# Performance work log

Measured on AMD Instinct MI355X. Metric: run time of the kernel, lower is better.

Reference implementation:

```python
import jax, jax.numpy as jnp
import numpy as np
from math import sqrt

DIM = 256
HEADS = 4
GROUPS = min(DIM // 4, 32)  # = 32
EPS = 1e-6


def setup_inputs() -> dict:
    key = jax.random.key(0)
    ks = jax.random.split(key, 10)
    B, C, H, W = 16, DIM, 32, 32
    x = jax.random.normal(ks[0], (B, C, H, W), dtype=jnp.float32)
    s = 1.0 / sqrt(C)
    inp = {
        'x': x,
        'gn_scale': jnp.ones((C,), jnp.float32),
        'gn_bias': jnp.zeros((C,), jnp.float32),
        'Wq': jax.random.normal(ks[1], (C, C), jnp.float32) * s,
        'bq': jnp.zeros((C,), jnp.float32),
        'Wk': jax.random.normal(ks[2], (C, C), jnp.float32) * s,
        'bk': jnp.zeros((C,), jnp.float32),
        'Wv': jax.random.normal(ks[3], (C, C), jnp.float32) * s,
        'bv': jnp.zeros((C,), jnp.float32),
        'Wp': jax.random.normal(ks[4], (C, C), jnp.float32) * s,
        'bp': jnp.zeros((C,), jnp.float32),
    }
    return inp


def _group_norm(x, scale, bias):
    B, C, H, W = x.shape
    xg = x.reshape(B, GROUPS, C // GROUPS, H, W)
    mean = xg.mean(axis=(2, 3, 4), keepdims=True)
    var = xg.var(axis=(2, 3, 4), keepdims=True)
    xg = (xg - mean) * jax.lax.rsqrt(var + EPS)
    x = xg.reshape(B, C, H, W)
    return x * scale[None, :, None, None] + bias[None, :, None, None]


def _lin_ch(x, W, b):
    # 1x1 conv / linear over channel dim: (B,C,H,W) x (C,Cout) -> (B,Cout,H,W)
    return jnp.einsum('bchw,cd->bdhw', x, W) + b[None, :, None, None]


def reference(x, gn_scale, gn_bias, Wq, bq, Wk, bk, Wv, bv, Wp, bp):
    B, C, H, W = x.shape
    dh = C // HEADS
    _x = _group_norm(x, gn_scale, gn_bias)
    q = _lin_ch(_x, Wq, bq).reshape(B, HEADS, dh, H, W)
    k = _lin_ch(_x, Wk, bk).reshape(B, HEADS, dh, H, W)
    v = _lin_ch(_x, Wv, bv).reshape(B, HEADS, dh, H, W)
    scores = jnp.einsum('bhdxy,bhdij->bhxyij', q, k) / sqrt(C)
    scores = scores.reshape(B, HEADS, H, W, H * W)
    weights = jax.nn.softmax(scores, axis=-1).reshape(B, HEADS, H, W, H, W)
    h = jnp.einsum('bhxyij,bhdij->bhdxy', weights, v).reshape(B, C, H, W)
    h = _lin_ch(h, Wp, bp)
    ret = (x + h) / sqrt(2.0)
    return ret
```

## Files before the change

kernel.cpp:

```cpp
#include <hip/hip_runtime.h>
#include <hip/hip_bf16.h>

#define BATCH 16
#define CH    256
#define HW    1024
#define NH    4
#define DH    64
#define NG    32
#define CPG   8
#define EPSV  1e-6f

#define QSCALE 0.090168440055558706f

typedef __bf16 bf16x8 __attribute__((ext_vector_type(8)));
typedef float  f32x4  __attribute__((ext_vector_type(4)));

__device__ __forceinline__ unsigned short f2bf(float f) {
    union { __hip_bfloat16 h; unsigned short u; } cv;
    cv.h = __float2bfloat16(f);
    return cv.u;
}

__device__ __forceinline__ unsigned int fbits(float f) {
    union { float f; unsigned int u; } cv; cv.f = f; return cv.u;
}

__device__ __forceinline__ void gld_lds16(const unsigned short* g, unsigned short* l) {
    __builtin_amdgcn_global_load_lds(
        (const __attribute__((address_space(1))) void*)g,
        (__attribute__((address_space(3))) void*)l, 16, 0, 0);
}

__global__ void prep_gn_kernel(const float* Wq, const float* Wk, const float* Wv,
                               const float* Wp, const float* bq, const float* bk,
                               const float* bv, unsigned short* wqkv_t,
                               unsigned short* wp_t, float* bqkv,
                               const float* x, const float* scale, const float* bias,
                               unsigned short* xn) {
    int t = threadIdx.x;
    if (blockIdx.x < 1024) {
        int idx = blockIdx.x * 256 + t;
        if (idx < 768 * 256) {
            int n = idx >> 8, c = idx & 255;
            const float* W = (n < 256) ? Wq : (n < 512) ? Wk : Wv;
            int d = n & 255;
            wqkv_t[idx] = f2bf(W[c * 256 + d]);
        } else {
            int j = idx - 768 * 256;
            int n = j >> 8, c = j & 255;
            wp_t[j] = f2bf(Wp[c * 256 + n]);
        }
        if (idx < 768)
            bqkv[idx] = (idx < 256) ? bq[idx] : (idx < 512) ? bk[idx - 256] : bv[idx - 512];
    } else {
        int bg = blockIdx.x - 1024;
        const float4* p = reinterpret_cast<const float4*>(x + (size_t)bg * (CPG * HW));
        float va[8][4];
        float s = 0.f, ss = 0.f;
#pragma unroll
        for (int k = 0; k < 8; k++) {
            float4 v = p[t + 256 * k];
            va[k][0] = v.x; va[k][1] = v.y; va[k][2] = v.z; va[k][3] = v.w;
            s += v.x + v.y + v.z + v.w;
            ss += v.x * v.x + v.y * v.y + v.z * v.z + v.w * v.w;
        }
        for (int o = 32; o; o >>= 1) { s += __shfl_down(s, o); ss += __shfl_down(ss, o); }
        __shared__ float as_[4], ass_[4];
        __shared__ float sA[8], sB[8];
        int w = t >> 6;
        if ((t & 63) == 0) { as_[w] = s; ass_[w] = ss; }
        __syncthreads();
        if (t < 8) {
            float S = as_[0] + as_[1] + as_[2] + as_[3];
            float SS = ass_[0] + ass_[1] + ass_[2] + ass_[3];
            float mean = S / (float)(CPG * HW);
            float var = SS / (float)(CPG * HW) - mean * mean;
            float rstd = rsqrtf(var + EPSV);
            int g = bg & 31;
            int c = g * CPG + t;
            float a = rstd * scale[c];
            sA[t] = a;
            sB[t] = bias[c] - mean * a;
        }
        __syncthreads();
        int b = bg >> 5, g = bg & 31;
        unsigned short* dst = xn + ((size_t)b * HW + t * 4) * CH + g * CPG;
#pragma unroll
        for (int pl = 0; pl < 4; pl++) {
            union { bf16x8 v8; __hip_bfloat162 h2[4]; } u;
#pragma unroll
            for (int c2 = 0; c2 < 4; c2++) {
                float v0 = fmaf(va[2 * c2][pl],     sA[2 * c2],     sB[2 * c2]);
                float v1 = fmaf(va[2 * c2 + 1][pl], sA[2 * c2 + 1], sB[2 * c2 + 1]);
                u.h2[c2] = __float22bfloat162_rn(float2{v0, v1});
            }
            *reinterpret_cast<bf16x8*>(dst + (size_t)pl * CH) = u.v8;
        }
    }
}

__global__ __launch_bounds__(256) void qkv_kernel(const unsigned short* xn,
        const unsigned short* wqkv_t, const float* bqkv,
        unsigned short* qb, unsigned short* kb, unsigned short* vb) {
    int t = threadIdx.x;
    int wv = t >> 6, lane = t & 63, quad = lane >> 4, ln = lane & 15;
    int wr = wv >> 1, wc = wv & 1;
    int m0 = blockIdx.x * 128 + wr * 64;
    int n0 = blockIdx.y * 128 + wc * 64;

    f32x4 acc[4][4] = {};
    for (int k0 = 0; k0 < CH; k0 += 32) {
        int koff = k0 + quad * 8;
        bf16x8 af[4], bfr[4];
#pragma unroll
        for (int i = 0; i < 4; i++)
            af[i] = *reinterpret_cast<const bf16x8*>(
                xn + (size_t)(m0 + i * 16 + ln) * CH + koff);
#pragma unroll
        for (int j = 0; j < 4; j++)
            bfr[j] = *reinterpret_cast<const bf16x8*>(
                wqkv_t + (size_t)(n0 + j * 16 + ln) * CH + koff);
#pragma unroll
        for (int i = 0; i < 4; i++)
#pragma unroll
            for (int j = 0; j < 4; j++)
                acc[i][j] = __builtin_amdgcn_mfma_f32_16x16x32_bf16(af[i], bfr[j], acc[i][j], 0, 0, 0);
    }
#pragma unroll
    for (int j = 0; j < 4; j++) {
        int n = n0 + j * 16 + ln;
        float bias = bqkv[n];
        int which = n >> 8;
        int dh_ = n & 255;
        int head = dh_ >> 6, d = dh_ & 63;
#pragma unroll
        for (int i = 0; i < 4; i++) {
            int mb = m0 + i * 16 + quad * 4;
            int bi = mb >> 10, p = mb & 1023;
            int bh = bi * NH + head;
            if (which < 2) {
                unsigned short* dst = (which == 0 ? qb : kb) + (size_t)bh * HW * DH;
                float sc = (which == 0) ? QSCALE : 1.0f;
#pragma unroll
                for (int r = 0; r < 4; r++)
                    dst[(size_t)(p + r) * DH + d] = f2bf((acc[i][j][r] + bias) * sc);
            } else {
                unsigned short* dst = vb + ((size_t)bh * DH + d) * HW + p;
                ushort4 pk4;
                pk4.x = f2bf(acc[i][j][0] + bias);
                pk4.y = f2bf(acc[i][j][1] + bias);
                pk4.z = f2bf(acc[i][j][2] + bias);
                pk4.w = f2bf(acc[i][j][3] + bias);
                *reinterpret_cast<ushort4*>(dst) = pk4;
            }
        }
    }
}

__global__ __launch_bounds__(256) void attn_kernel(const unsigned short* qb,
        const unsigned short* kb, const unsigned short* vb, unsigned short* h_t) {
    int qblk = blockIdx.x, bh = blockIdx.y;
    int t = threadIdx.x;
    int wv = t >> 6, lane = t & 63, quad = lane >> 4, ln = lane & 15;
    int q0 = qblk * 128 + wv * 32;

    const unsigned short* Q = qb + (size_t)bh * HW * DH;
    const unsigned short* K = kb + (size_t)bh * HW * DH;
    const unsigned short* V = vb + (size_t)bh * DH * HW;

    __shared__ __align__(16) unsigned short kbuf[2][4096];
    __shared__ __align__(16) unsigned short vbuf[2][4096];
    __shared__ __align__(16) unsigned short pbuf[4][2][16][72];

    int c_a = wv * 64 + lane;
    int c_b = 256 + wv * 64 + lane;
    int pa = c_a >> 3, ja = (c_a & 7) ^ (pa & 7);
    int pb = c_b >> 3, jb = (c_b & 7) ^ (pb & 7);
    const unsigned short* pka = K + (size_t)pa * DH + ja * 8;
    const unsigned short* pkb = K + (size_t)pb * DH + jb * 8;
    const unsigned short* pva = V + (size_t)pa * HW + ja * 8;
    const unsigned short* pvb = V + (size_t)pb * HW + jb * 8;
    int lofs_a = wv * 512, lofs_b = 2048 + wv * 512;

    int koffs[4][2];
#pragma unroll
    for (int mt = 0; mt < 4; mt++) {
        int p = mt * 16 + ln, sw = p & 7;
#pragma unroll
        for (int kk = 0; kk < 2; kk++)
            koffs[mt][kk] = p * 64 + (((kk * 4 + quad) ^ sw) * 8);
    }

    bf16x8 qf[2][2];
#pragma unroll
    for (int nq = 0; nq < 2; nq++)
#pragma unroll
        for (int kk = 0; kk < 2; kk++)
            qf[nq][kk] = *reinterpret_cast<const bf16x8*>(
                Q + (size_t)(q0 + nq * 16 + ln) * DH + kk * 32 + quad * 8);

    f32x4 ls[2] = {};
    f32x4 o[2][4] = {};

    gld_lds16(pka, &kbuf[0][lofs_a]);
    gld_lds16(pkb, &kbuf[0][lofs_b]);
    gld_lds16(pva, &vbuf[0][lofs_a]);
    gld_lds16(pvb, &vbuf[0][lofs_b]);
    pka += 64 * DH; pkb += 64 * DH; pva += 64; pvb += 64;

#define ATTN_TILE(B, DO_STAGE)                                                      \
    {                                                                               \
        __syncthreads();                                                            \
        if (DO_STAGE) {                                                             \
            gld_lds16(pka, &kbuf[B ^ 1][lofs_a]);                                   \
            gld_lds16(pkb, &kbuf[B ^ 1][lofs_b]);                                   \
            gld_lds16(pva, &vbuf[B ^ 1][lofs_a]);                                   \
            gld_lds16(pvb, &vbuf[B ^ 1][lofs_b]);                                   \
            pka += 64 * DH; pkb += 64 * DH; pva += 64; pvb += 64;                   \
        }                                                                           \
        bf16x8 kf[4][2], vf[4][2];                                                  \
        _Pragma("unroll")                                                           \
        for (int mt = 0; mt < 4; mt++) {                                            \
            _Pragma("unroll")                                                       \
            for (int kk = 0; kk < 2; kk++) {                                        \
                kf[mt][kk] = *reinterpret_cast<const bf16x8*>(&kbuf[B][koffs[mt][kk]]); \
                vf[mt][kk] = *reinterpret_cast<const bf16x8*>(&vbuf[B][koffs[mt][kk]]); \
            }                                                                       \
        }                                                                           \
        f32x4 s[2][4] = {};                                                         \
        _Pragma("unroll")                                                           \
        for (int nq = 0; nq < 2; nq++)                                              \
            _Pragma("unroll")                                                       \
            for (int mt = 0; mt < 4; mt++) {                                        \
                s[nq][mt] = __builtin_amdgcn_mfma_f32_16x16x32_bf16(kf[mt][0], qf[nq][0], s[nq][mt], 0, 0, 0); \
                s[nq][mt] = __builtin_amdgcn_mfma_f32_16x16x32_bf16(kf[mt][1], qf[nq][1], s[nq][mt], 0, 0, 0); \
            }                                                                       \
        _Pragma("unroll")                                                           \
        for (int nq = 0; nq < 2; nq++)                                              \
            _Pragma("unroll")                                                       \
            for (int mt = 0; mt < 4; mt++) {                                        \
                float e0 = __builtin_amdgcn_exp2f(s[nq][mt][0]);                    \
                float e1 = __builtin_amdgcn_exp2f(s[nq][mt][1]);                    \
                float e2 = __builtin_amdgcn_exp2f(s[nq][mt][2]);                    \
                float e3 = __builtin_amdgcn_exp2f(s[nq][mt][3]);                    \
                ls[nq][0] += e0; ls[nq][1] += e1;                                   \
                ls[nq][2] += e2; ls[nq][3] += e3;                                   \
                uint2 pk2;                                                          \
                pk2.x = __builtin_amdgcn_perm(fbits(e1), fbits(e0), 0x07060302u);   \
                pk2.y = __builtin_amdgcn_perm(fbits(e3), fbits(e2), 0x07060302u);   \
                *reinterpret_cast<uint2*>(&pbuf[wv][nq][ln][mt * 16 + quad * 4]) = pk2; \
            }                                                                       \
        _Pragma("unroll")                                                           \
        for (int nq = 0; nq < 2; nq++)                                              \
            _Pragma("unroll")                                                       \
            for (int kk = 0; kk < 2; kk++) {                                        \
                bf16x8 pf = *reinterpret_cast<const bf16x8*>(&pbuf[wv][nq][ln][kk * 32 + quad * 8]); \
                _Pragma("unroll")                                                   \
                for (int mt = 0; mt < 4; mt++)                                      \
                    o[nq][mt] = __builtin_amdgcn_mfma_f32_16x16x32_bf16(vf[mt][kk], pf, o[nq][mt], 0, 0, 0); \
            }                                                                       \
    }

    for (int u = 0; u < 8; u++) {
        ATTN_TILE(0, true)
        ATTN_TILE(1, (u < 7))
    }
#undef ATTN_TILE

    int b_ = bh >> 2, head = bh & 3;
#pragma unroll
    for (int nq = 0; nq < 2; nq++) {
        float lsum = ls[nq][0] + ls[nq][1] + ls[nq][2] + ls[nq][3];
        lsum += __shfl_xor(lsum, 16);
        lsum += __shfl_xor(lsum, 32);
        float inv = 1.0f / lsum;
        unsigned short* dst = h_t + ((size_t)b_ * HW + q0 + nq * 16 + ln) * CH + head * DH;
#pragma unroll
        for (int mt = 0; mt < 4; mt++) {
            ushort4 pk4;
            pk4.x = f2bf(o[nq][mt][0] * inv);
            pk4.y = f2bf(o[nq][mt][1] * inv);
            pk4.z = f2bf(o[nq][mt][2] * inv);
            pk4.w = f2bf(o[nq][mt][3] * inv);
            *reinterpret_cast<ushort4*>(dst + mt * 16 + quad * 4) = pk4;
        }
    }
}

__global__ __launch_bounds__(256) void proj_kernel(const unsigned short* h_t,
        const unsigned short* wp_t, const float* bp, const float* x, float* out) {
    int t = threadIdx.x;
    int wv = t >> 6, lane = t & 63, quad = lane >> 4, ln = lane & 15;
    int wr = wv >> 1, wc = wv & 1;
    int m0 = blockIdx.x * 64 + wr * 32;
    int n0 = blockIdx.y * 128 + wc * 64;

    f32x4 acc[2][4] = {};
    for (int k0 = 0; k0 < CH; k0 += 32) {
        int koff = k0 + quad * 8;
        bf16x8 af[2], bfr[4];
#pragma unroll
        for (int i = 0; i < 2; i++)
            af[i] = *reinterpret_cast<const bf16x8*>(h_t + (size_t)(m0 + i * 16 + ln) * CH + koff);
#pragma unroll
        for (int j = 0; j < 4; j++)
            bfr[j] = *reinterpret_cast<const bf16x8*>(wp_t + (size_t)(n0 + j * 16 + ln) * CH + koff);
#pragma unroll
        for (int i = 0; i < 2; i++)
#pragma unroll
            for (int j = 0; j < 4; j++)
                acc[i][j] = __builtin_amdgcn_mfma_f32_16x16x32_bf16(af[i], bfr[j], acc[i][j], 0, 0, 0);
    }
    const float inv_s2 = 0.70710678118654752440f;
#pragma unroll
    for (int j = 0; j < 4; j++) {
        int n = n0 + j * 16 + ln;
        float bias = bp[n];
#pragma unroll
        for (int i = 0; i < 2; i++) {
            int mb = m0 + i * 16 + quad * 4;
            int bi = mb >> 10, p = mb & 1023;
            size_t off = ((size_t)(bi * CH + n)) * HW + p;
            float4 xv = *reinterpret_cast<const float4*>(x + off);
            float4 ov;
            ov.x = (xv.x + acc[i][j][0] + bias) * inv_s2;
            ov.y = (xv.y + acc[i][j][1] + bias) * inv_s2;
            ov.z = (xv.z + acc[i][j][2] + bias) * inv_s2;
            ov.w = (xv.w + acc[i][j][3] + bias) * inv_s2;
            *reinterpret_cast<float4*>(out + off) = ov;
        }
    }
}

extern "C" void kernel_launch(void* const* d_in, const int* in_sizes, int n_in,
                              void* d_out, int out_size, void* d_ws, size_t ws_size,
                              hipStream_t stream) {
    const float* x        = (const float*)d_in[0];
    const float* gn_scale = (const float*)d_in[1];
    const float* gn_bias  = (const float*)d_in[2];
    const float* Wq = (const float*)d_in[3];
    const float* bq = (const float*)d_in[4];
    const float* Wk = (const float*)d_in[5];
    const float* bk = (const float*)d_in[6];
    const float* Wv = (const float*)d_in[7];
    const float* bv = (const float*)d_in[8];
    const float* Wp = (const float*)d_in[9];
    const float* bp = (const float*)d_in[10];
    float* out = (float*)d_out;

    char* ws = (char*)d_ws;
    float*          bqkv   = (float*)(ws + 0);
    unsigned short* wqkv_t = (unsigned short*)(ws + 36864);
    unsigned short* wp_t   = (unsigned short*)(ws + 430080);
    unsigned short* xn     = (unsigned short*)(ws + 1048576);
    unsigned short* h_t    = (unsigned short*)(ws + 9437184);
    unsigned short* qb     = (unsigned short*)(ws + 17825792);
    unsigned short* kb     = (unsigned short*)(ws + 26214400);
    unsigned short* vb     = (unsigned short*)(ws + 34603008);

    prep_gn_kernel<<<1536, 256, 0, stream>>>(Wq, Wk, Wv, Wp, bq, bk, bv,
                                             wqkv_t, wp_t, bqkv,
                                             x, gn_scale, gn_bias, xn);
    qkv_kernel<<<dim3(128, 6), 256, 0, stream>>>(xn, wqkv_t, bqkv, qb, kb, vb);
    attn_kernel<<<dim3(8, 64), 256, 0, stream>>>(qb, kb, vb, h_t);
    proj_kernel<<<dim3(256, 2), 256, 0, stream>>>(h_t, wp_t, bp, x, out);
}
```

Baseline: 165.4 us.

## Load K/V fragments directly from global into registers, dropping LDS staging

Removes the shared-memory double buffer for K and V tiles that was filled with global_load_lds, and instead has each lane load its bf16x8 MFMA fragments straight from global memory. K fragments for the next tile are prefetched into a second register set; V fragments are loaded per tile. This removes the per-tile __syncthreads and the LDS round trip, but each of the four waves now fetches the full K/V tiles separately, relying on L1/L2 for reuse. It also raises register pressure.

```diff
diff --git a/kernel.cpp b/kernel.cpp
--- a/kernel.cpp
+++ b/kernel.cpp
@@ -23,12 +23,6 @@
 
 __device__ __forceinline__ unsigned int fbits(float f) {
     union { float f; unsigned int u; } cv; cv.f = f; return cv.u;
-}
-
-__device__ __forceinline__ void gld_lds16(const unsigned short* g, unsigned short* l) {
-    __builtin_amdgcn_global_load_lds(
-        (const __attribute__((address_space(1))) void*)g,
-        (__attribute__((address_space(3))) void*)l, 16, 0, 0);
 }
 
 __global__ void prep_gn_kernel(const float* Wq, const float* Wk, const float* Wv,
@@ -168,28 +162,10 @@
     const unsigned short* K = kb + (size_t)bh * HW * DH;
     const unsigned short* V = vb + (size_t)bh * DH * HW;
 
-    __shared__ __align__(16) unsigned short kbuf[2][4096];
-    __shared__ __align__(16) unsigned short vbuf[2][4096];
     __shared__ __align__(16) unsigned short pbuf[4][2][16][72];
 
-    int c_a = wv * 64 + lane;
-    int c_b = 256 + wv * 64 + lane;
-    int pa = c_a >> 3, ja = (c_a & 7) ^ (pa & 7);
-    int pb = c_b >> 3, jb = (c_b & 7) ^ (pb & 7);
-    const unsigned short* pka = K + (size_t)pa * DH + ja * 8;
-    const unsigned short* pkb = K + (size_t)pb * DH + jb * 8;
-    const unsigned short* pva = V + (size_t)pa * HW + ja * 8;
-    const unsigned short* pvb = V + (size_t)pb * HW + jb * 8;
-    int lofs_a = wv * 512, lofs_b = 2048 + wv * 512;
-
-    int koffs[4][2];
-#pragma unroll
-    for (int mt = 0; mt < 4; mt++) {
-        int p = mt * 16 + ln, sw = p & 7;
-#pragma unroll
-        for (int kk = 0; kk < 2; kk++)
-            koffs[mt][kk] = p * 64 + (((kk * 4 + quad) ^ sw) * 8);
-    }
+    const unsigned short* Kp = K + (size_t)ln * DH + quad * 8;
+    const unsigned short* Vp = V + (size_t)ln * HW + quad * 8;
 
     bf16x8 qf[2][2];
 #pragma unroll
@@ -202,38 +178,39 @@
     f32x4 ls[2] = {};
     f32x4 o[2][4] = {};
 
-    gld_lds16(pka, &kbuf[0][lofs_a]);
-    gld_lds16(pkb, &kbuf[0][lofs_b]);
-    gld_lds16(pva, &vbuf[0][lofs_a]);
-    gld_lds16(pvb, &vbuf[0][lofs_b]);
-    pka += 64 * DH; pkb += 64 * DH; pva += 64; pvb += 64;
-
-#define ATTN_TILE(B, DO_STAGE)                                                      \
+    bf16x8 kfA[4][2], kfB[4][2];
+#pragma unroll
+    for (int mt = 0; mt < 4; mt++)
+#pragma unroll
+        for (int kk = 0; kk < 2; kk++)
+            kfA[mt][kk] = *reinterpret_cast<const bf16x8*>(
+                Kp + (size_t)(mt * 16) * DH + kk * 32);
+
+#define ATTN_TILE(CUR, NXT, TILE, DO_PF)                                            \
     {                                                                               \
-        __syncthreads();                                                            \
-        if (DO_STAGE) {                                                             \
-            gld_lds16(pka, &kbuf[B ^ 1][lofs_a]);                                   \
-            gld_lds16(pkb, &kbuf[B ^ 1][lofs_b]);                                   \
-            gld_lds16(pva, &vbuf[B ^ 1][lofs_a]);                                   \
-            gld_lds16(pvb, &vbuf[B ^ 1][lofs_b]);                                   \
-            pka += 64 * DH; pkb += 64 * DH; pva += 64; pvb += 64;                   \
-        }                                                                           \
-        bf16x8 kf[4][2], vf[4][2];                                                  \
+        int t64 = (TILE) * 64;                                                      \
+        bf16x8 vf[4][2];                                                            \
         _Pragma("unroll")                                                           \
-        for (int mt = 0; mt < 4; mt++) {                                            \
-            _Pragma("unroll")                                                       \
-            for (int kk = 0; kk < 2; kk++) {                                        \
-                kf[mt][kk] = *reinterpret_cast<const bf16x8*>(&kbuf[B][koffs[mt][kk]]); \
-                vf[mt][kk] = *reinterpret_cast<const bf16x8*>(&vbuf[B][koffs[mt][kk]]); \
-            }                                                                       \
+        for (int mt = 0; mt < 4; mt++)                                              \
+            _Pragma("unroll")                                                       \
+            for (int kk = 0; kk < 2; kk++)                                          \
+                vf[mt][kk] = *reinterpret_cast<const bf16x8*>(                      \
+                    Vp + (size_t)(mt * 16) * HW + t64 + kk * 32);                   \
+        if (DO_PF) {                                                                \
+            _Pragma("unroll")                                                       \
+            for (int mt = 0; mt < 4; mt++)                                          \
+                _Pragma("unroll")                                                   \
+                for (int kk = 0; kk < 2; kk++)                                      \
+                    NXT[mt][kk] = *reinterpret_cast<const bf16x8*>(                 \
+                        Kp + (size_t)(t64 + 64 + mt * 16) * DH + kk * 32);          \
         }                                                                           \
         f32x4 s[2][4] = {};                                                         \
         _Pragma("unroll")                                                           \
         for (int nq = 0; nq < 2; nq++)                                              \
             _Pragma("unroll")                                                       \
             for (int mt = 0; mt < 4; mt++) {                                        \
-                s[nq][mt] = __builtin_amdgcn_mfma_f32_16x16x32_bf16(kf[mt][0], qf[nq][0], s[nq][mt], 0, 0, 0); \
-                s[nq][mt] = __builtin_amdgcn_mfma_f32_16x16x32_bf16(kf[mt][1], qf[nq][1], s[nq][mt], 0, 0, 0); \
+                s[nq][mt] = __builtin_amdgcn_mfma_f32_16x16x32_bf16(CUR[mt][0], qf[nq][0], s[nq][mt], 0, 0, 0); \
+                s[nq][mt] = __builtin_amdgcn_mfma_f32_16x16x32_bf16(CUR[mt][1], qf[nq][1], s[nq][mt], 0, 0, 0); \
             }                                                                       \
         _Pragma("unroll")                                                           \
         for (int nq = 0; nq < 2; nq++)                                              \
@@ -262,8 +239,8 @@
     }
 
     for (int u = 0; u < 8; u++) {
-        ATTN_TILE(0, true)
-        ATTN_TILE(1, (u < 7))
+        ATTN_TILE(kfA, kfB, 2 * u,     true)
+        ATTN_TILE(kfB, kfA, 2 * u + 1, (u < 7))
     }
 #undef ATTN_TILE
 
```

Result: slower. 196.4 us (+18.7%).

## Shrink attention blocks to two waves and tile weight transpose through LDS

Applied to the files above, without the earlier changes.

The attention kernel now runs 128-thread blocks covering 64 queries each, so the grid doubles to 1024 blocks. Each wave issues four K/V staging loads per tile, and the P buffer is reused per query subtile to cut LDS use. Separately, the weight transpose/convert prep now goes through a padded LDS tile with coalesced reads and vectorized bf16 writes in 32 blocks instead of 1024 scattered-read blocks. The smaller attention blocks aim for better occupancy and load balance, at the cost of loading K/V twice as often per query.

```diff
diff --git a/kernel.cpp b/kernel.cpp
--- a/kernel.cpp
+++ b/kernel.cpp
@@ -38,22 +38,34 @@
                                const float* x, const float* scale, const float* bias,
                                unsigned short* xn) {
     int t = threadIdx.x;
-    if (blockIdx.x < 1024) {
-        int idx = blockIdx.x * 256 + t;
-        if (idx < 768 * 256) {
-            int n = idx >> 8, c = idx & 255;
-            const float* W = (n < 256) ? Wq : (n < 512) ? Wk : Wv;
-            int d = n & 255;
-            wqkv_t[idx] = f2bf(W[c * 256 + d]);
-        } else {
-            int j = idx - 768 * 256;
-            int n = j >> 8, c = j & 255;
-            wp_t[j] = f2bf(Wp[c * 256 + n]);
-        }
-        if (idx < 768)
-            bqkv[idx] = (idx < 256) ? bq[idx] : (idx < 512) ? bk[idx - 256] : bv[idx - 512];
+    int blk = blockIdx.x;
+    if (blk < 32) {
+        __shared__ float lt[256][33];
+        int w = blk >> 3, c0 = (blk & 7) * 32;
+        const float* W = (w == 0) ? Wq : (w == 1) ? Wk : (w == 2) ? Wv : Wp;
+#pragma unroll
+        for (int i = 0; i < 32; i++)
+            lt[t][i] = W[(size_t)(c0 + i) * 256 + t];
+        __syncthreads();
+        unsigned short* orow = (w < 3) ? (wqkv_t + ((size_t)(w * 256 + t)) * 256 + c0)
+                                       : (wp_t + (size_t)t * 256 + c0);
+#pragma unroll
+        for (int s8 = 0; s8 < 4; s8++) {
+            union { bf16x8 v8; __hip_bfloat162 h2[4]; } u;
+#pragma unroll
+            for (int e = 0; e < 4; e++) {
+                float v0 = lt[t][s8 * 8 + 2 * e];
+                float v1 = lt[t][s8 * 8 + 2 * e + 1];
+                u.h2[e] = __float22bfloat162_rn(float2{v0, v1});
+            }
+            *reinterpret_cast<bf16x8*>(orow + s8 * 8) = u.v8;
+        }
+    } else if (blk == 32) {
+        bqkv[t]       = bq[t];
+        bqkv[256 + t] = bk[t];
+        bqkv[512 + t] = bv[t];
     } else {
-        int bg = blockIdx.x - 1024;
+        int bg = blk - 33;
         const float4* p = reinterpret_cast<const float4*>(x + (size_t)bg * (CPG * HW));
         float va[8][4];
         float s = 0.f, ss = 0.f;
@@ -157,12 +169,12 @@
     }
 }
 
-__global__ __launch_bounds__(256) void attn_kernel(const unsigned short* qb,
+__global__ __launch_bounds__(128) void attn_kernel(const unsigned short* qb,
         const unsigned short* kb, const unsigned short* vb, unsigned short* h_t) {
     int qblk = blockIdx.x, bh = blockIdx.y;
     int t = threadIdx.x;
     int wv = t >> 6, lane = t & 63, quad = lane >> 4, ln = lane & 15;
-    int q0 = qblk * 128 + wv * 32;
+    int q0 = qblk * 64 + wv * 32;
 
     const unsigned short* Q = qb + (size_t)bh * HW * DH;
     const unsigned short* K = kb + (size_t)bh * HW * DH;
@@ -170,17 +182,30 @@
 
     __shared__ __align__(16) unsigned short kbuf[2][4096];
     __shared__ __align__(16) unsigned short vbuf[2][4096];
-    __shared__ __align__(16) unsigned short pbuf[4][2][16][72];
-
-    int c_a = wv * 64 + lane;
-    int c_b = 256 + wv * 64 + lane;
-    int pa = c_a >> 3, ja = (c_a & 7) ^ (pa & 7);
-    int pb = c_b >> 3, jb = (c_b & 7) ^ (pb & 7);
-    const unsigned short* pka = K + (size_t)pa * DH + ja * 8;
-    const unsigned short* pkb = K + (size_t)pb * DH + jb * 8;
-    const unsigned short* pva = V + (size_t)pa * HW + ja * 8;
-    const unsigned short* pvb = V + (size_t)pb * HW + jb * 8;
-    int lofs_a = wv * 512, lofs_b = 2048 + wv * 512;
+    __shared__ __align__(16) unsigned short pbuf[2][16][72];
+
+    const unsigned short* pka[4];
+    const unsigned short* pva[4];
+    int lofs[4];
+#pragma unroll
+    for (int i = 0; i < 4; i++) {
+        int c = (2 * i + wv) * 64 + lane;
+        int p = c >> 3, j = (c & 7) ^ (p & 7);
+        pka[i] = K + (size_t)p * DH + j * 8;
+        pva[i] = V + (size_t)p * HW + j * 8;
+        lofs[i] = (2 * i + wv) * 512;
+    }
+
+#define STAGE(B)                                                                    \
+    {                                                                               \
+        _Pragma("unroll")                                                           \
+        for (int i = 0; i < 4; i++) {                                               \
+            gld_lds16(pka[i], &kbuf[B][lofs[i]]);                                   \
+            gld_lds16(pva[i], &vbuf[B][lofs[i]]);                                   \
+        }                                                                           \
+        _Pragma("unroll")                                                           \
+        for (int i = 0; i < 4; i++) { pka[i] += 64 * DH; pva[i] += 64; }            \
+    }
 
     int koffs[4][2];
 #pragma unroll
@@ -202,22 +227,12 @@
     f32x4 ls[2] = {};
     f32x4 o[2][4] = {};
 
-    gld_lds16(pka, &kbuf[0][lofs_a]);
-    gld_lds16(pkb, &kbuf[0][lofs_b]);
-    gld_lds16(pva, &vbuf[0][lofs_a]);
-    gld_lds16(pvb, &vbuf[0][lofs_b]);
-    pka += 64 * DH; pkb += 64 * DH; pva += 64; pvb += 64;
+    STAGE(0)
 
 #define ATTN_TILE(B, DO_STAGE)                                                      \
     {                                                                               \
         __syncthreads();                                                            \
-        if (DO_STAGE) {                                                             \
-            gld_lds16(pka, &kbuf[B ^ 1][lofs_a]);                                   \
-            gld_lds16(pkb, &kbuf[B ^ 1][lofs_b]);                                   \
-            gld_lds16(pva, &vbuf[B ^ 1][lofs_a]);                                   \
-            gld_lds16(pvb, &vbuf[B ^ 1][lofs_b]);                                   \
-            pka += 64 * DH; pkb += 64 * DH; pva += 64; pvb += 64;                   \
-        }                                                                           \
+        if (DO_STAGE) STAGE(B ^ 1)                                                  \
         bf16x8 kf[4][2], vf[4][2];                                                  \
         _Pragma("unroll")                                                           \
         for (int mt = 0; mt < 4; mt++) {                                            \
@@ -236,7 +251,7 @@
                 s[nq][mt] = __builtin_amdgcn_mfma_f32_16x16x32_bf16(kf[mt][1], qf[nq][1], s[nq][mt], 0, 0, 0); \
             }                                                                       \
         _Pragma("unroll")                                                           \
-        for (int nq = 0; nq < 2; nq++)                                              \
+        for (int nq = 0; nq < 2; nq++) {                                            \
             _Pragma("unroll")                                                       \
             for (int mt = 0; mt < 4; mt++) {                                        \
                 float e0 = __builtin_amdgcn_exp2f(s[nq][mt][0]);                    \
@@ -248,17 +263,16 @@
                 uint2 pk2;                                                          \
                 pk2.x = __builtin_amdgcn_perm(fbits(e1), fbits(e0), 0x07060302u);   \
                 pk2.y = __builtin_amdgcn_perm(fbits(e3), fbits(e2), 0x07060302u);   \
-                *reinterpret_cast<uint2*>(&pbuf[wv][nq][ln][mt * 16 + quad * 4]) = pk2; \
+                *reinterpret_cast<uint2*>(&pbuf[wv][ln][mt * 16 + quad * 4]) = pk2; \
             }                                                                       \
-        _Pragma("unroll")                                                           \
-        for (int nq = 0; nq < 2; nq++)                                              \
             _Pragma("unroll")                                                       \
             for (int kk = 0; kk < 2; kk++) {                                        \
-                bf16x8 pf = *reinterpret_cast<const bf16x8*>(&pbuf[wv][nq][ln][kk * 32 + quad * 8]); \
+                bf16x8 pf = *reinterpret_cast<const bf16x8*>(&pbuf[wv][ln][kk * 32 + quad * 8]); \
                 _Pragma("unroll")                                                   \
                 for (int mt = 0; mt < 4; mt++)                                      \
                     o[nq][mt] = __builtin_amdgcn_mfma_f32_16x16x32_bf16(vf[mt][kk], pf, o[nq][mt], 0, 0, 0); \
             }                                                                       \
+        }                                                                           \
     }
 
     for (int u = 0; u < 8; u++) {
@@ -266,6 +280,7 @@
         ATTN_TILE(1, (u < 7))
     }
 #undef ATTN_TILE
+#undef STAGE
 
     int b_ = bh >> 2, head = bh & 3;
 #pragma unroll
@@ -358,10 +373,10 @@
     unsigned short* kb     = (unsigned short*)(ws + 26214400);
     unsigned short* vb     = (unsigned short*)(ws + 34603008);
 
-    prep_gn_kernel<<<1536, 256, 0, stream>>>(Wq, Wk, Wv, Wp, bq, bk, bv,
-                                             wqkv_t, wp_t, bqkv,
-                                             x, gn_scale, gn_bias, xn);
+    prep_gn_kernel<<<545, 256, 0, stream>>>(Wq, Wk, Wv, Wp, bq, bk, bv,
+                                            wqkv_t, wp_t, bqkv,
+                                            x, gn_scale, gn_bias, xn);
     qkv_kernel<<<dim3(128, 6), 256, 0, stream>>>(xn, wqkv_t, bqkv, qb, kb, vb);
-    attn_kernel<<<dim3(8, 64), 256, 0, stream>>>(qb, kb, vb, h_t);
+    attn_kernel<<<dim3(16, 64), 128, 0, stream>>>(qb, kb, vb, h_t);
     proj_kernel<<<dim3(256, 2), 256, 0, stream>>>(h_t, wp_t, bp, x, out);
 }
```

Result: no change. 167.2 us (+1.1%).
